# Kernel optimization log

Hardware: AMD Instinct MI355X
Metric: run time of the kernel (lower is better)

The kernel has to match this reference:

```python
import jax, jax.numpy as jnp
import numpy as np

NUM_GRAPHS = 2048


def gcn_conv(x, W, b, edge, N):
    # PyG GCNConv: x' = D^{-1/2} (A + I) D^{-1/2} (x W) + b
    src, dst = edge[0], edge[1]
    loop = jnp.arange(N, dtype=src.dtype)
    src = jnp.concatenate([src, loop])
    dst = jnp.concatenate([dst, loop])
    h = x @ W  # [N, out]
    deg = jax.ops.segment_sum(jnp.ones(dst.shape, x.dtype), dst, num_segments=N)
    dinv = jnp.where(deg > 0, jax.lax.rsqrt(deg), 0.0)
    norm = dinv[src] * dinv[dst]  # [E+N]
    out = jax.ops.segment_sum(h[src] * norm[:, None], dst, num_segments=N)
    return out + b


def pool_max_mean(x, batch, G):
    mx = jax.ops.segment_max(x, batch, num_segments=G)
    mx = jnp.where(jnp.isfinite(mx), mx, 0.0)  # guard empty segments
    s = jax.ops.segment_sum(x, batch, num_segments=G)
    cnt = jax.ops.segment_sum(jnp.ones((x.shape[0],), x.dtype), batch, num_segments=G)
    mean = s / jnp.maximum(cnt, 1.0)[:, None]
    return mx, mean


def setup_inputs() -> dict:
    key = jax.random.key(0)
    ks = jax.random.split(key, 20)
    F, CE, SE, DD = 64, 64, 32, 128
    Nc, Ec, Ns, Es = 100000, 1250000, 100000, 1250000

    def glorot(k, shape):
        fan_in, fan_out = shape[0], shape[1]
        lim = np.sqrt(6.0 / (fan_in + fan_out)).astype(np.float32)
        return jax.random.uniform(k, shape, jnp.float32, -lim, lim)

    inp = {
        "c": jax.random.normal(ks[0], (Nc, F), jnp.float32),
        "c_edge": jax.random.randint(ks[1], (2, Ec), 0, Nc),
        "c_batch": jnp.sort(jax.random.randint(ks[2], (Nc,), 0, NUM_GRAPHS)),
        "s": jax.random.normal(ks[3], (Ns, F), jnp.float32),
        "s_edge": jax.random.randint(ks[4], (2, Es), 0, Ns),
        "s_batch": jnp.sort(jax.random.randint(ks[5], (Ns,), 0, NUM_GRAPHS)),
        "Wc0": glorot(ks[6], (F, CE)), "bc0": jnp.zeros((CE,), jnp.float32),
        "Wc1": glorot(ks[7], (CE, CE)), "bc1": jnp.zeros((CE,), jnp.float32),
        "Wc2": glorot(ks[8], (CE, CE)), "bc2": jnp.zeros((CE,), jnp.float32),
        "Ws0": glorot(ks[9], (F, SE)), "bs0": jnp.zeros((SE,), jnp.float32),
        "Ws1": glorot(ks[10], (SE, SE)), "bs1": jnp.zeros((SE,), jnp.float32),
        "Ws2": glorot(ks[11], (SE, SE)), "bs2": jnp.zeros((SE,), jnp.float32),
        "Wd": glorot(ks[12], ((CE + SE) * 2, DD)), "bd": jnp.zeros((DD,), jnp.float32),
        "Wo": glorot(ks[13], (DD, 1)), "bo": jnp.zeros((1,), jnp.float32),
    }
    return inp


def reference(c, c_edge, c_batch, s, s_edge, s_batch,
              Wc0, bc0, Wc1, bc1, Wc2, bc2,
              Ws0, bs0, Ws1, bs1, Ws2, bs2,
              Wd, bd, Wo, bo):
    Nc, Ns = c.shape[0], s.shape[0]
    cro = jax.nn.relu(gcn_conv(c, Wc0, bc0, c_edge, Nc))
    cro = jax.nn.relu(gcn_conv(cro, Wc1, bc1, c_edge, Nc))
    cro = jax.nn.relu(gcn_conv(cro, Wc2, bc2, c_edge, Nc))
    solv = jax.nn.relu(gcn_conv(s, Ws0, bs0, s_edge, Ns))
    solv = jax.nn.relu(gcn_conv(solv, Ws1, bs1, s_edge, Ns))
    solv = jax.nn.relu(gcn_conv(solv, Ws2, bs2, s_edge, Ns))
    c_mx, c_mean = pool_max_mean(cro, c_batch, NUM_GRAPHS)
    s_mx, s_mean = pool_max_mean(solv, s_batch, NUM_GRAPHS)
    embed = jnp.concatenate([c_mx, c_mean, s_mx, s_mean], axis=1)  # [G, 192]
    dense = jax.nn.relu(embed @ Wd + bd)
    out = dense @ Wo + bo  # [G, 1]
    return out, embed
```

## Files before the change

kernel.cpp:

```cpp
#include <hip/hip_runtime.h>
#include <hip/hip_fp16.h>
#include <math.h>


static inline int cdiv(int a, int b) { return (a + b - 1) / b; }

#define BUCKET_CAP 8192
#define P1_CHUNK   4096

typedef _Float16 v8h __attribute__((ext_vector_type(8)));
typedef float    v4f __attribute__((ext_vector_type(4)));

__global__ void zero_int(int* __restrict__ p, int n) {
    int i = blockIdx.x * blockDim.x + threadIdx.x;
    if (i < n) p[i] = 0;
}

__global__ __launch_bounds__(256) void p1_partition(const int* __restrict__ c_edge, int Ec,
                                                    const int* __restrict__ s_edge, int Es,
                                                    int Nc_pad, int Etot, int nbuck,
                                                    int* __restrict__ bucket_fill,
                                                    unsigned* __restrict__ pk) {
    __shared__ unsigned       wbuf[P1_CHUNK];
    __shared__ unsigned short bbuf[P1_CHUNK];
    __shared__ int            hist[512];
    int e0 = blockIdx.x * P1_CHUNK;
    int n  = Etot - e0;
    if (n > P1_CHUNK) n = P1_CHUNK;
    for (int i = threadIdx.x; i < nbuck; i += 256) hist[i] = 0;
    __syncthreads();
    for (int i = threadIdx.x; i < n; i += 256) {
        int e = e0 + i, src, g;
        if (e < Ec) { src = c_edge[e]; g = c_edge[Ec + e]; }
        else        { int e2 = e - Ec; src = s_edge[e2]; g = Nc_pad + s_edge[Es + e2]; }
        int b   = g >> 9;
        wbuf[i] = ((unsigned)(g & 511) << 17) | (unsigned)src;
        bbuf[i] = (unsigned short)b;
        atomicAdd(&hist[b], 1);
    }
    __syncthreads();
    for (int i = threadIdx.x; i < nbuck; i += 256) {
        int h = hist[i];
        hist[i] = h ? atomicAdd(&bucket_fill[i], h) : 0;
    }
    __syncthreads();
    for (int i = threadIdx.x; i < n; i += 256) {
        int b    = bbuf[i];
        int slot = atomicAdd(&hist[b], 1);
        if (slot < BUCKET_CAP) pk[(size_t)b * BUCKET_CAP + slot] = wbuf[i];
    }
}

__global__ __launch_bounds__(512) void p2_scanbuckets(const int* __restrict__ fill, int nbuck,
                                                      int* __restrict__ basearr,
                                                      int* __restrict__ off_all, int Ntot_pad, int Etot) {
    __shared__ int sh[512];
    int v = (threadIdx.x < nbuck) ? fill[threadIdx.x] : 0;
    sh[threadIdx.x] = v;
    __syncthreads();
    for (int ofs = 1; ofs < 512; ofs <<= 1) {
        int t = (threadIdx.x >= ofs) ? sh[threadIdx.x - ofs] : 0;
        __syncthreads();
        sh[threadIdx.x] += t;
        __syncthreads();
    }
    if (threadIdx.x < nbuck) basearr[threadIdx.x] = sh[threadIdx.x] - v;
    if (threadIdx.x == 0) off_all[Ntot_pad] = Etot;
}

__global__ __launch_bounds__(512) void p3_build(const unsigned* __restrict__ pk,
                                                const int* __restrict__ fillarr,
                                                const int* __restrict__ basearr,
                                                int* __restrict__ off_all,
                                                float* __restrict__ dinv,
                                                int* __restrict__ csr) {
    __shared__ int sh[512];
    int b    = blockIdx.x;
    int fill = fillarr[b];
    if (fill > BUCKET_CAP) fill = BUCKET_CAP;
    int base = basearr[b];
    const unsigned* reg = pk + (size_t)b * BUCKET_CAP;
    sh[threadIdx.x] = 0;
    __syncthreads();
    for (int i = threadIdx.x; i < fill; i += 512) atomicAdd(&sh[reg[i] >> 17], 1);
    __syncthreads();
    int cnt = sh[threadIdx.x];
    for (int ofs = 1; ofs < 512; ofs <<= 1) {
        int t = (threadIdx.x >= ofs) ? sh[threadIdx.x - ofs] : 0;
        __syncthreads();
        sh[threadIdx.x] += t;
        __syncthreads();
    }
    int excl = sh[threadIdx.x] - cnt;
    int node = b * 512 + threadIdx.x;
    off_all[node] = base + excl;
    dinv[node]    = rsqrtf((float)(cnt + 1));
    __syncthreads();
    sh[threadIdx.x] = excl;
    __syncthreads();
    for (int i = threadIdx.x; i < fill; i += 512) {
        unsigned w    = reg[i];
        int      slot = atomicAdd(&sh[w >> 17], 1);
        csr[base + slot] = (int)(w & 0x1FFFFu);
    }
}

template <int K, int M, typename TIN>
__device__ void gemm_mfma(int bid, const TIN* __restrict__ X, const float* __restrict__ W,
                          const float* __restrict__ dinv, __half* __restrict__ H, int N,
                          char* smem_) {
    constexpr int RB = 64;
    constexpr int KP = K + 8;
    constexpr int NT = M / 16;
    constexpr int KS = K / 32;
    _Float16* Xh = (_Float16*)smem_;
    _Float16* Wz = Xh + RB * KP;
    const int t    = threadIdx.x;
    const int row0 = bid * RB;

    constexpr int WENT = NT * KS * 64;
    for (int idx = t; idx < WENT; idx += 256) {
        int lane = idx & 63, rest = idx >> 6;
        int ks = rest % KS, ntl = rest / KS;
        int kbase = ks * 32 + (lane >> 4) * 8;
        int col   = ntl * 16 + (lane & 15);
        union { float4 f4; _Float16 h[8]; } u;
#pragma unroll
        for (int j = 0; j < 8; ++j) u.h[j] = (_Float16)W[(kbase + j) * M + col];
        *(float4*)(Wz + idx * 8) = u.f4;
    }
    if constexpr (sizeof(TIN) == 4) {
        constexpr int NI = RB * K / 4;
        for (int idx = t; idx < NI; idx += 256) {
            int row = idx / (K / 4), k4 = idx % (K / 4);
            int gr = row0 + row;
            float4 v = make_float4(0.f, 0.f, 0.f, 0.f);
            if (gr < N) v = *(const float4*)((const float*)X + (size_t)gr * K + k4 * 4);
            union { float2 f2; _Float16 h[4]; } u;
            u.h[0] = (_Float16)v.x; u.h[1] = (_Float16)v.y;
            u.h[2] = (_Float16)v.z; u.h[3] = (_Float16)v.w;
            *(float2*)(Xh + row * KP + k4 * 4) = u.f2;
        }
    } else {
        constexpr int NI = RB * K / 8;
        for (int idx = t; idx < NI; idx += 256) {
            int row = idx / (K / 8), k8 = idx % (K / 8);
            int gr = row0 + row;
            float4 v = make_float4(0.f, 0.f, 0.f, 0.f);
            if (gr < N) v = *(const float4*)((const __half*)X + (size_t)gr * K + k8 * 8);
            *(float4*)(Xh + row * KP + k8 * 8) = v;
        }
    }
    __syncthreads();

    const int wave = t >> 6, lane = t & 63;
    const int quad = lane >> 4, nl = lane & 15;
    const int rowA = wave * 16 + nl;

    v4f acc[NT];
#pragma unroll
    for (int i = 0; i < NT; ++i) acc[i] = (v4f){0.f, 0.f, 0.f, 0.f};

#pragma unroll
    for (int ks = 0; ks < KS; ++ks) {
        v8h a = *(const v8h*)(Xh + rowA * KP + ks * 32 + quad * 8);
#pragma unroll
        for (int ntl = 0; ntl < NT; ++ntl) {
            v8h b = *(const v8h*)(Wz + ((ntl * KS + ks) * 64 + lane) * 8);
            acc[ntl] = __builtin_amdgcn_mfma_f32_16x16x32_f16(a, b, acc[ntl], 0, 0, 0);
        }
    }

#pragma unroll
    for (int r = 0; r < 4; ++r) {
        int gr = row0 + wave * 16 + quad * 4 + r;
        if (gr < N) {
            float dv = dinv[gr];
#pragma unroll
            for (int ntl = 0; ntl < NT; ++ntl)
                H[(size_t)gr * M + ntl * 16 + nl] = __float2half(acc[ntl][r] * dv);
        }
    }
}

__device__ __forceinline__ float4 load4h(const float2* __restrict__ base, size_t idx) {
    float2 r = base[idx];
    union { float2 f2; __half2 h2[2]; } u;
    u.f2 = r;
    float2 a = __half22float2(u.h2[0]);
    float2 b = __half22float2(u.h2[1]);
    return make_float4(a.x, a.y, b.x, b.y);
}

template <int M>
__device__ void agg_body(int bid, const __half* __restrict__ H,
                         const int* __restrict__ off_g,
                         const int* __restrict__ csr,
                         const float* __restrict__ dinv_g,
                         const float* __restrict__ b,
                         __half* __restrict__ out, int Nloc) {
    constexpr int L   = M / 4;
    constexpr int NPW = 64 / L;
    int lane = threadIdx.x & 63;
    int wave = threadIdx.x >> 6;
    int fq   = lane & (L - 1);
    int sub  = lane / L;
    int node = (bid * 4 + wave) * NPW + sub;
    if (node >= Nloc) return;
    const float2* H4 = (const float2*)H;
    int j0 = off_g[node], j1 = off_g[node + 1];
    float4 acc = load4h(H4, (size_t)node * L + fq);
    int j = j0;
    for (; j + 8 <= j1; j += 8) {
        int s0 = csr[j],     s1 = csr[j + 1], s2 = csr[j + 2], s3 = csr[j + 3];
        int s4 = csr[j + 4], s5 = csr[j + 5], s6 = csr[j + 6], s7 = csr[j + 7];
        float4 a0 = load4h(H4, (size_t)s0 * L + fq);
        float4 a1 = load4h(H4, (size_t)s1 * L + fq);
        float4 a2 = load4h(H4, (size_t)s2 * L + fq);
        float4 a3 = load4h(H4, (size_t)s3 * L + fq);
        float4 a4 = load4h(H4, (size_t)s4 * L + fq);
        float4 a5 = load4h(H4, (size_t)s5 * L + fq);
        float4 a6 = load4h(H4, (size_t)s6 * L + fq);
        float4 a7 = load4h(H4, (size_t)s7 * L + fq);
        acc.x += (a0.x + a1.x + a2.x + a3.x) + (a4.x + a5.x + a6.x + a7.x);
        acc.y += (a0.y + a1.y + a2.y + a3.y) + (a4.y + a5.y + a6.y + a7.y);
        acc.z += (a0.z + a1.z + a2.z + a3.z) + (a4.z + a5.z + a6.z + a7.z);
        acc.w += (a0.w + a1.w + a2.w + a3.w) + (a4.w + a5.w + a6.w + a7.w);
    }
    for (; j + 4 <= j1; j += 4) {
        int s0 = csr[j], s1 = csr[j + 1], s2 = csr[j + 2], s3 = csr[j + 3];
        float4 a0 = load4h(H4, (size_t)s0 * L + fq);
        float4 a1 = load4h(H4, (size_t)s1 * L + fq);
        float4 a2 = load4h(H4, (size_t)s2 * L + fq);
        float4 a3 = load4h(H4, (size_t)s3 * L + fq);
        acc.x += a0.x + a1.x + a2.x + a3.x;
        acc.y += a0.y + a1.y + a2.y + a3.y;
        acc.z += a0.z + a1.z + a2.z + a3.z;
        acc.w += a0.w + a1.w + a2.w + a3.w;
    }
    for (; j < j1; ++j) {
        float4 a = load4h(H4, (size_t)csr[j] * L + fq);
        acc.x += a.x; acc.y += a.y; acc.z += a.z; acc.w += a.w;
    }
    float  dv = dinv_g[node];
    float4 bb = ((const float4*)b)[fq];
    float  vx = dv * acc.x + bb.x;
    float  vy = dv * acc.y + bb.y;
    float  vz = dv * acc.z + bb.z;
    float  vw = dv * acc.w + bb.w;
    union { float2 f2; __half2 h2[2]; } o;
    o.h2[0] = __floats2half2_rn(vx > 0.f ? vx : 0.f, vy > 0.f ? vy : 0.f);
    o.h2[1] = __floats2half2_rn(vz > 0.f ? vz : 0.f, vw > 0.f ? vw : 0.f);
    ((float2*)out)[(size_t)node * L + fq] = o.f2;
}

__global__ __launch_bounds__(256) void gemmBoth0(const float* __restrict__ Xc, const float* __restrict__ Wc,
                                                 __half* __restrict__ cH, int Nc,
                                                 const float* __restrict__ Xs, const float* __restrict__ Ws,
                                                 __half* __restrict__ sH, int Ns,
                                                 const float* __restrict__ dinv_all, int Nc_pad, int nbC) {
    __shared__ __align__(16) char smem[17408];
    if (blockIdx.x < nbC) gemm_mfma<64, 64, float>(blockIdx.x, Xc, Wc, dinv_all, cH, Nc, smem);
    else                  gemm_mfma<64, 32, float>(blockIdx.x - nbC, Xs, Ws, dinv_all + Nc_pad, sH, Ns, smem);
}

__global__ __launch_bounds__(256) void gemmBoth(const __half* __restrict__ Xc, const float* __restrict__ Wc,
                                                __half* __restrict__ cH, int Nc,
                                                const __half* __restrict__ Xs, const float* __restrict__ Ws,
                                                __half* __restrict__ sH, int Ns,
                                                const float* __restrict__ dinv_all, int Nc_pad, int nbC) {
    __shared__ __align__(16) char smem[17408];
    if (blockIdx.x < nbC) gemm_mfma<64, 64, __half>(blockIdx.x, Xc, Wc, dinv_all, cH, Nc, smem);
    else                  gemm_mfma<32, 32, __half>(blockIdx.x - nbC, Xs, Ws, dinv_all + Nc_pad, sH, Ns, smem);
}

__global__ __launch_bounds__(256) void aggBoth(const __half* __restrict__ cH, const __half* __restrict__ sH,
                                               const int* __restrict__ off_all, const int* __restrict__ csr_all,
                                               const float* __restrict__ dinv_all,
                                               const float* __restrict__ bc, const float* __restrict__ bs,
                                               __half* __restrict__ outc, __half* __restrict__ outs,
                                               int Nc, int Ns, int Nc_pad, int nbC) {
    if (blockIdx.x < nbC)
        agg_body<64>(blockIdx.x, cH, off_all, csr_all, dinv_all, bc, outc, Nc);
    else
        agg_body<32>(blockIdx.x - nbC, sH, off_all + Nc_pad, csr_all,
                     dinv_all + Nc_pad, bs, outs, Ns);
}

__device__ __forceinline__ int lbound(const int* __restrict__ a, int n, int key) {
    int lo = 0, hi = n;
    while (lo < hi) {
        int mid = (lo + hi) >> 1;
        if (a[mid] < key) lo = mid + 1; else hi = mid;
    }
    return lo;
}

__global__ __launch_bounds__(128) void poolDense(const __half* __restrict__ cX, const int* __restrict__ c_batch, int Nc,
                                                 const __half* __restrict__ sX, const int* __restrict__ s_batch, int Ns,
                                                 const float* __restrict__ Wd, const float* __restrict__ bd,
                                                 const float* __restrict__ Wo, const float* __restrict__ bo,
                                                 float* __restrict__ outv, float* __restrict__ embed) {
    __shared__ float e[192];
    __shared__ float red[128];
    int g = blockIdx.x, t = threadIdx.x;
    if (t < 64) {
        int lo = lbound(c_batch, Nc, g), hi = lbound(c_batch, Nc, g + 1);
        float mx = 0.f, sm = 0.f;
        for (int i = lo; i < hi; ++i) {
            float v = __half2float(cX[(size_t)i * 64 + t]);
            mx = fmaxf(mx, v); sm += v;
        }
        int cn = hi - lo;
        e[t]      = mx;
        e[64 + t] = sm / (float)(cn > 0 ? cn : 1);
    } else if (t < 96) {
        int f  = t - 64;
        int lo = lbound(s_batch, Ns, g), hi = lbound(s_batch, Ns, g + 1);
        float mx = 0.f, sm = 0.f;
        for (int i = lo; i < hi; ++i) {
            float v = __half2float(sX[(size_t)i * 32 + f]);
            mx = fmaxf(mx, v); sm += v;
        }
        int cn = hi - lo;
        e[128 + f] = mx;
        e[160 + f] = sm / (float)(cn > 0 ? cn : 1);
    }
    __syncthreads();
    for (int k = t; k < 192; k += 128) embed[(size_t)g * 192 + k] = e[k];
    float acc = bd[t];
    for (int k = 0; k < 192; ++k) acc += e[k] * Wd[k * 128 + t];
    float d = acc > 0.f ? acc : 0.f;
    red[t]  = d * Wo[t];
    __syncthreads();
    for (int ofs = 64; ofs > 0; ofs >>= 1) {
        if (t < ofs) red[t] += red[t + ofs];
        __syncthreads();
    }
    if (t == 0) outv[g] = red[0] + bo[0];
}


extern "C" void kernel_launch(void* const* d_in, const int* in_sizes, int n_in,
                              void* d_out, int out_size, void* d_ws, size_t ws_size,
                              hipStream_t stream) {
    const float* c       = (const float*)d_in[0];
    const int*   c_edge  = (const int*)d_in[1];
    const int*   c_batch = (const int*)d_in[2];
    const float* s       = (const float*)d_in[3];
    const int*   s_edge  = (const int*)d_in[4];
    const int*   s_batch = (const int*)d_in[5];
    const float* Wc0 = (const float*)d_in[6],  *bc0 = (const float*)d_in[7];
    const float* Wc1 = (const float*)d_in[8],  *bc1 = (const float*)d_in[9];
    const float* Wc2 = (const float*)d_in[10], *bc2 = (const float*)d_in[11];
    const float* Ws0 = (const float*)d_in[12], *bs0 = (const float*)d_in[13];
    const float* Ws1 = (const float*)d_in[14], *bs1 = (const float*)d_in[15];
    const float* Ws2 = (const float*)d_in[16], *bs2 = (const float*)d_in[17];
    const float* Wd  = (const float*)d_in[18], *bd  = (const float*)d_in[19];
    const float* Wo  = (const float*)d_in[20], *bo  = (const float*)d_in[21];

    const int Nc = in_sizes[0] / 64;
    const int Ec = in_sizes[1] / 2;
    const int Ns = in_sizes[3] / 64;
    const int Es = in_sizes[4] / 2;
    const int G  = out_size / 193;
    const int Nc_pad   = cdiv(Nc, 512) * 512;
    const int Ns_pad   = cdiv(Ns, 512) * 512;
    const int Ntot_pad = Nc_pad + Ns_pad;
    const int Etot     = Ec + Es;
    const int nbuck    = Ntot_pad >> 9;

    char* p = (char*)d_ws;
    auto  alloc = [&](size_t bytes) -> void* {
        void* r = (void*)p;
        p += (bytes + 255) & ~(size_t)255;
        return r;
    };
    int*      bucket_fill = (int*)alloc(512 * 4);
    int*      bucket_base = (int*)alloc(512 * 4);
    unsigned* pk          = (unsigned*)alloc((size_t)nbuck * BUCKET_CAP * 4);
    int*      off_all     = (int*)alloc(((size_t)Ntot_pad + 1) * 4);
    int*      csr_all     = (int*)alloc((size_t)Etot * 4);
    float*    dinv_all    = (float*)alloc((size_t)Ntot_pad * 4);
    __half*   bufC        = (__half*)alloc((size_t)Nc * 64 * 2);
    __half*   bufS        = (__half*)alloc((size_t)Ns * 32 * 2);
    __half*   cH          = (__half*)alloc((size_t)Nc * 64 * 2);
    __half*   sH          = (__half*)alloc((size_t)Ns * 32 * 2);

    float* outv  = (float*)d_out;
    float* embed = outv + G;

    const int nbGmC = cdiv(Nc, 64), nbGmS = cdiv(Ns, 64);
    const int nbAgC = Nc_pad / 16,  nbAgS = Ns_pad / 32;

    zero_int<<<cdiv(nbuck, 256), 256, 0, stream>>>(bucket_fill, nbuck);
    p1_partition<<<cdiv(Etot, P1_CHUNK), 256, 0, stream>>>(c_edge, Ec, s_edge, Es,
                                                           Nc_pad, Etot, nbuck, bucket_fill, pk);
    p2_scanbuckets<<<1, 512, 0, stream>>>(bucket_fill, nbuck, bucket_base, off_all, Ntot_pad, Etot);
    p3_build<<<nbuck, 512, 0, stream>>>(pk, bucket_fill, bucket_base,
                                        off_all, dinv_all, csr_all);

    gemmBoth0<<<nbGmC + nbGmS, 256, 0, stream>>>(c, Wc0, cH, Nc, s, Ws0, sH, Ns,
                                                 dinv_all, Nc_pad, nbGmC);
    aggBoth<<<nbAgC + nbAgS, 256, 0, stream>>>(cH, sH, off_all, csr_all, dinv_all,
                                               bc0, bs0, bufC, bufS, Nc, Ns, Nc_pad, nbAgC);
    gemmBoth<<<nbGmC + nbGmS, 256, 0, stream>>>(bufC, Wc1, cH, Nc, bufS, Ws1, sH, Ns,
                                                dinv_all, Nc_pad, nbGmC);
    aggBoth<<<nbAgC + nbAgS, 256, 0, stream>>>(cH, sH, off_all, csr_all, dinv_all,
                                               bc1, bs1, bufC, bufS, Nc, Ns, Nc_pad, nbAgC);
    gemmBoth<<<nbGmC + nbGmS, 256, 0, stream>>>(bufC, Wc2, cH, Nc, bufS, Ws2, sH, Ns,
                                                dinv_all, Nc_pad, nbGmC);
    aggBoth<<<nbAgC + nbAgS, 256, 0, stream>>>(cH, sH, off_all, csr_all, dinv_all,
                                               bc2, bs2, bufC, bufS, Nc, Ns, Nc_pad, nbAgC);

    poolDense<<<G, 128, 0, stream>>>(bufC, c_batch, Nc, bufS, s_batch, Ns,
                                     Wd, bd, Wo, bo, outv, embed);
}
```

Measured before the change: 367.6 us.

## Fold bucket scan into CSR build and widen aggregation gathers to 16 bytes

The single-block bucket prefix scan kernel is removed, and every p3_build block now recomputes the bucket scan itself, saving one launch and its serialization at the cost of redundant scan work per block. The aggregation kernel switches from 8-byte to 16-byte half-precision gathers: each lane handles 8 features, so fewer lanes serve each node and more nodes fit per wave. The grid sizes are halved to match. The 8-way unrolled neighbor loop is dropped in favour of a 4-way loop, which lowers memory-level parallelism per lane but fits the wider loads.

```diff
diff --git a/kernel.cpp b/kernel.cpp
--- a/kernel.cpp
+++ b/kernel.cpp
@@ -51,54 +51,51 @@
     }
 }
 
-__global__ __launch_bounds__(512) void p2_scanbuckets(const int* __restrict__ fill, int nbuck,
-                                                      int* __restrict__ basearr,
-                                                      int* __restrict__ off_all, int Ntot_pad, int Etot) {
-    __shared__ int sh[512];
-    int v = (threadIdx.x < nbuck) ? fill[threadIdx.x] : 0;
-    sh[threadIdx.x] = v;
-    __syncthreads();
-    for (int ofs = 1; ofs < 512; ofs <<= 1) {
-        int t = (threadIdx.x >= ofs) ? sh[threadIdx.x - ofs] : 0;
-        __syncthreads();
-        sh[threadIdx.x] += t;
-        __syncthreads();
-    }
-    if (threadIdx.x < nbuck) basearr[threadIdx.x] = sh[threadIdx.x] - v;
-    if (threadIdx.x == 0) off_all[Ntot_pad] = Etot;
-}
-
 __global__ __launch_bounds__(512) void p3_build(const unsigned* __restrict__ pk,
                                                 const int* __restrict__ fillarr,
-                                                const int* __restrict__ basearr,
+                                                int nbuck, int Ntot_pad, int Etot,
                                                 int* __restrict__ off_all,
                                                 float* __restrict__ dinv,
                                                 int* __restrict__ csr) {
     __shared__ int sh[512];
-    int b    = blockIdx.x;
-    int fill = fillarr[b];
+    int b = blockIdx.x, tid = threadIdx.x;
+
+    int fv = (tid < nbuck) ? fillarr[tid] : 0;
+    sh[tid] = fv;
+    __syncthreads();
+    for (int ofs = 1; ofs < 512; ofs <<= 1) {
+        int t = (tid >= ofs) ? sh[tid - ofs] : 0;
+        __syncthreads();
+        sh[tid] += t;
+        __syncthreads();
+    }
+    int fill_b = fillarr[b];
+    int base   = sh[b] - fill_b;
+    if (b == 0 && tid == 0) off_all[Ntot_pad] = Etot;
+    int fill = fill_b;
     if (fill > BUCKET_CAP) fill = BUCKET_CAP;
-    int base = basearr[b];
     const unsigned* reg = pk + (size_t)b * BUCKET_CAP;
-    sh[threadIdx.x] = 0;
-    __syncthreads();
-    for (int i = threadIdx.x; i < fill; i += 512) atomicAdd(&sh[reg[i] >> 17], 1);
-    __syncthreads();
-    int cnt = sh[threadIdx.x];
+    __syncthreads();
+
+    sh[tid] = 0;
+    __syncthreads();
+    for (int i = tid; i < fill; i += 512) atomicAdd(&sh[reg[i] >> 17], 1);
+    __syncthreads();
+    int cnt = sh[tid];
     for (int ofs = 1; ofs < 512; ofs <<= 1) {
-        int t = (threadIdx.x >= ofs) ? sh[threadIdx.x - ofs] : 0;
+        int t = (tid >= ofs) ? sh[tid - ofs] : 0;
         __syncthreads();
-        sh[threadIdx.x] += t;
+        sh[tid] += t;
         __syncthreads();
     }
-    int excl = sh[threadIdx.x] - cnt;
-    int node = b * 512 + threadIdx.x;
+    int excl = sh[tid] - cnt;
+    int node = b * 512 + tid;
     off_all[node] = base + excl;
     dinv[node]    = rsqrtf((float)(cnt + 1));
     __syncthreads();
-    sh[threadIdx.x] = excl;
-    __syncthreads();
-    for (int i = threadIdx.x; i < fill; i += 512) {
+    sh[tid] = excl;
+    __syncthreads();
+    for (int i = tid; i < fill; i += 512) {
         unsigned w    = reg[i];
         int      slot = atomicAdd(&sh[w >> 17], 1);
         csr[base + slot] = (int)(w & 0x1FFFFu);
@@ -109,10 +106,7 @@
 __device__ void gemm_mfma(int bid, const TIN* __restrict__ X, const float* __restrict__ W,
                           const float* __restrict__ dinv, __half* __restrict__ H, int N,
                           char* smem_) {
-    constexpr int RB = 64;
-    constexpr int KP = K + 8;
-    constexpr int NT = M / 16;
-    constexpr int KS = K / 32;
+    constexpr int RB = 64, KP = K + 8, NT = M / 16, KS = K / 32;
     _Float16* Xh = (_Float16*)smem_;
     _Float16* Wz = Xh + RB * KP;
     const int t    = threadIdx.x;
@@ -160,7 +154,6 @@
     v4f acc[NT];
 #pragma unroll
     for (int i = 0; i < NT; ++i) acc[i] = (v4f){0.f, 0.f, 0.f, 0.f};
-
 #pragma unroll
     for (int ks = 0; ks < KS; ++ks) {
         v8h a = *(const v8h*)(Xh + rowA * KP + ks * 32 + quad * 8);
@@ -170,7 +163,6 @@
             acc[ntl] = __builtin_amdgcn_mfma_f32_16x16x32_f16(a, b, acc[ntl], 0, 0, 0);
         }
     }
-
 #pragma unroll
     for (int r = 0; r < 4; ++r) {
         int gr = row0 + wave * 16 + quad * 4 + r;
@@ -183,23 +175,28 @@
     }
 }
 
-__device__ __forceinline__ float4 load4h(const float2* __restrict__ base, size_t idx) {
-    float2 r = base[idx];
-    union { float2 f2; __half2 h2[2]; } u;
-    u.f2 = r;
-    float2 a = __half22float2(u.h2[0]);
-    float2 b = __half22float2(u.h2[1]);
-    return make_float4(a.x, a.y, b.x, b.y);
+__device__ __forceinline__ void cvt8h(float4 r, float4& lo, float4& hi) {
+    union { float4 f4; __half2 h2[4]; } u;
+    u.f4 = r;
+    float2 p0 = __half22float2(u.h2[0]);
+    float2 p1 = __half22float2(u.h2[1]);
+    float2 p2 = __half22float2(u.h2[2]);
+    float2 p3 = __half22float2(u.h2[3]);
+    lo = make_float4(p0.x, p0.y, p1.x, p1.y);
+    hi = make_float4(p2.x, p2.y, p3.x, p3.y);
+}
+
+__device__ __forceinline__ void add8(float4& alo, float4& ahi, float4 r4lo, float4 r4hi) {
+    alo.x += r4lo.x; alo.y += r4lo.y; alo.z += r4lo.z; alo.w += r4lo.w;
+    ahi.x += r4hi.x; ahi.y += r4hi.y; ahi.z += r4hi.z; ahi.w += r4hi.w;
 }
 
 template <int M>
 __device__ void agg_body(int bid, const __half* __restrict__ H,
-                         const int* __restrict__ off_g,
-                         const int* __restrict__ csr,
-                         const float* __restrict__ dinv_g,
-                         const float* __restrict__ b,
+                         const int* __restrict__ off_g, const int* __restrict__ csr,
+                         const float* __restrict__ dinv_g, const float* __restrict__ b,
                          __half* __restrict__ out, int Nloc) {
-    constexpr int L   = M / 4;
+    constexpr int L = M / 8;
     constexpr int NPW = 64 / L;
     int lane = threadIdx.x & 63;
     int wave = threadIdx.x >> 6;
@@ -207,51 +204,45 @@
     int sub  = lane / L;
     int node = (bid * 4 + wave) * NPW + sub;
     if (node >= Nloc) return;
-    const float2* H4 = (const float2*)H;
+    const float4* H8 = (const float4*)H;
     int j0 = off_g[node], j1 = off_g[node + 1];
-    float4 acc = load4h(H4, (size_t)node * L + fq);
+    float4 alo, ahi;
+    cvt8h(H8[(size_t)node * L + fq], alo, ahi);
     int j = j0;
-    for (; j + 8 <= j1; j += 8) {
-        int s0 = csr[j],     s1 = csr[j + 1], s2 = csr[j + 2], s3 = csr[j + 3];
-        int s4 = csr[j + 4], s5 = csr[j + 5], s6 = csr[j + 6], s7 = csr[j + 7];
-        float4 a0 = load4h(H4, (size_t)s0 * L + fq);
-        float4 a1 = load4h(H4, (size_t)s1 * L + fq);
-        float4 a2 = load4h(H4, (size_t)s2 * L + fq);
-        float4 a3 = load4h(H4, (size_t)s3 * L + fq);
-        float4 a4 = load4h(H4, (size_t)s4 * L + fq);
-        float4 a5 = load4h(H4, (size_t)s5 * L + fq);
-        float4 a6 = load4h(H4, (size_t)s6 * L + fq);
-        float4 a7 = load4h(H4, (size_t)s7 * L + fq);
-        acc.x += (a0.x + a1.x + a2.x + a3.x) + (a4.x + a5.x + a6.x + a7.x);
-        acc.y += (a0.y + a1.y + a2.y + a3.y) + (a4.y + a5.y + a6.y + a7.y);
-        acc.z += (a0.z + a1.z + a2.z + a3.z) + (a4.z + a5.z + a6.z + a7.z);
-        acc.w += (a0.w + a1.w + a2.w + a3.w) + (a4.w + a5.w + a6.w + a7.w);
-    }
     for (; j + 4 <= j1; j += 4) {
         int s0 = csr[j], s1 = csr[j + 1], s2 = csr[j + 2], s3 = csr[j + 3];
-        float4 a0 = load4h(H4, (size_t)s0 * L + fq);
-        float4 a1 = load4h(H4, (size_t)s1 * L + fq);
-        float4 a2 = load4h(H4, (size_t)s2 * L + fq);
-        float4 a3 = load4h(H4, (size_t)s3 * L + fq);
-        acc.x += a0.x + a1.x + a2.x + a3.x;
-        acc.y += a0.y + a1.y + a2.y + a3.y;
-        acc.z += a0.z + a1.z + a2.z + a3.z;
-        acc.w += a0.w + a1.w + a2.w + a3.w;
+        float4 r0 = H8[(size_t)s0 * L + fq];
+        float4 r1 = H8[(size_t)s1 * L + fq];
+        float4 r2 = H8[(size_t)s2 * L + fq];
+        float4 r3 = H8[(size_t)s3 * L + fq];
+        float4 lo, hi;
+        cvt8h(r0, lo, hi); add8(alo, ahi, lo, hi);
+        cvt8h(r1, lo, hi); add8(alo, ahi, lo, hi);
+        cvt8h(r2, lo, hi); add8(alo, ahi, lo, hi);
+        cvt8h(r3, lo, hi); add8(alo, ahi, lo, hi);
     }
     for (; j < j1; ++j) {
-        float4 a = load4h(H4, (size_t)csr[j] * L + fq);
-        acc.x += a.x; acc.y += a.y; acc.z += a.z; acc.w += a.w;
-    }
-    float  dv = dinv_g[node];
-    float4 bb = ((const float4*)b)[fq];
-    float  vx = dv * acc.x + bb.x;
-    float  vy = dv * acc.y + bb.y;
-    float  vz = dv * acc.z + bb.z;
-    float  vw = dv * acc.w + bb.w;
-    union { float2 f2; __half2 h2[2]; } o;
-    o.h2[0] = __floats2half2_rn(vx > 0.f ? vx : 0.f, vy > 0.f ? vy : 0.f);
-    o.h2[1] = __floats2half2_rn(vz > 0.f ? vz : 0.f, vw > 0.f ? vw : 0.f);
-    ((float2*)out)[(size_t)node * L + fq] = o.f2;
+        float4 lo, hi;
+        cvt8h(H8[(size_t)csr[j] * L + fq], lo, hi);
+        add8(alo, ahi, lo, hi);
+    }
+    float  dv  = dinv_g[node];
+    const float4* b4 = (const float4*)b;
+    float4 blo = b4[2 * fq], bhi = b4[2 * fq + 1];
+    float v0 = fmaxf(dv * alo.x + blo.x, 0.f);
+    float v1 = fmaxf(dv * alo.y + blo.y, 0.f);
+    float v2 = fmaxf(dv * alo.z + blo.z, 0.f);
+    float v3 = fmaxf(dv * alo.w + blo.w, 0.f);
+    float v4 = fmaxf(dv * ahi.x + bhi.x, 0.f);
+    float v5 = fmaxf(dv * ahi.y + bhi.y, 0.f);
+    float v6 = fmaxf(dv * ahi.z + bhi.z, 0.f);
+    float v7 = fmaxf(dv * ahi.w + bhi.w, 0.f);
+    union { float4 f4; __half2 h2[4]; } o;
+    o.h2[0] = __floats2half2_rn(v0, v1);
+    o.h2[1] = __floats2half2_rn(v2, v3);
+    o.h2[2] = __floats2half2_rn(v4, v5);
+    o.h2[3] = __floats2half2_rn(v6, v7);
+    ((float4*)out)[(size_t)node * L + fq] = o.f4;
 }
 
 __global__ __launch_bounds__(256) void gemmBoth0(const float* __restrict__ Xc, const float* __restrict__ Wc,
@@ -377,40 +368,38 @@
         return r;
     };
     int*      bucket_fill = (int*)alloc(512 * 4);
-    int*      bucket_base = (int*)alloc(512 * 4);
     unsigned* pk          = (unsigned*)alloc((size_t)nbuck * BUCKET_CAP * 4);
     int*      off_all     = (int*)alloc(((size_t)Ntot_pad + 1) * 4);
     int*      csr_all     = (int*)alloc((size_t)Etot * 4);
     float*    dinv_all    = (float*)alloc((size_t)Ntot_pad * 4);
     __half*   bufC        = (__half*)alloc((size_t)Nc * 64 * 2);
     __half*   bufS        = (__half*)alloc((size_t)Ns * 32 * 2);
-    __half*   cH          = (__half*)alloc((size_t)Nc * 64 * 2);
-    __half*   sH          = (__half*)alloc((size_t)Ns * 32 * 2);
+    __half*   cHa         = (__half*)alloc((size_t)Nc * 64 * 2);
+    __half*   sHa         = (__half*)alloc((size_t)Ns * 32 * 2);
 
     float* outv  = (float*)d_out;
     float* embed = outv + G;
 
     const int nbGmC = cdiv(Nc, 64), nbGmS = cdiv(Ns, 64);
-    const int nbAgC = Nc_pad / 16,  nbAgS = Ns_pad / 32;
+    const int nbAgC = Nc_pad / 32,  nbAgS = Ns_pad / 64;
 
     zero_int<<<cdiv(nbuck, 256), 256, 0, stream>>>(bucket_fill, nbuck);
     p1_partition<<<cdiv(Etot, P1_CHUNK), 256, 0, stream>>>(c_edge, Ec, s_edge, Es,
                                                            Nc_pad, Etot, nbuck, bucket_fill, pk);
-    p2_scanbuckets<<<1, 512, 0, stream>>>(bucket_fill, nbuck, bucket_base, off_all, Ntot_pad, Etot);
-    p3_build<<<nbuck, 512, 0, stream>>>(pk, bucket_fill, bucket_base,
+    p3_build<<<nbuck, 512, 0, stream>>>(pk, bucket_fill, nbuck, Ntot_pad, Etot,
                                         off_all, dinv_all, csr_all);
 
-    gemmBoth0<<<nbGmC + nbGmS, 256, 0, stream>>>(c, Wc0, cH, Nc, s, Ws0, sH, Ns,
+    gemmBoth0<<<nbGmC + nbGmS, 256, 0, stream>>>(c, Wc0, cHa, Nc, s, Ws0, sHa, Ns,
                                                  dinv_all, Nc_pad, nbGmC);
-    aggBoth<<<nbAgC + nbAgS, 256, 0, stream>>>(cH, sH, off_all, csr_all, dinv_all,
+    aggBoth<<<nbAgC + nbAgS, 256, 0, stream>>>(cHa, sHa, off_all, csr_all, dinv_all,
                                                bc0, bs0, bufC, bufS, Nc, Ns, Nc_pad, nbAgC);
-    gemmBoth<<<nbGmC + nbGmS, 256, 0, stream>>>(bufC, Wc1, cH, Nc, bufS, Ws1, sH, Ns,
+    gemmBoth<<<nbGmC + nbGmS, 256, 0, stream>>>(bufC, Wc1, cHa, Nc, bufS, Ws1, sHa, Ns,
                                                 dinv_all, Nc_pad, nbGmC);
-    aggBoth<<<nbAgC + nbAgS, 256, 0, stream>>>(cH, sH, off_all, csr_all, dinv_all,
+    aggBoth<<<nbAgC + nbAgS, 256, 0, stream>>>(cHa, sHa, off_all, csr_all, dinv_all,
                                                bc1, bs1, bufC, bufS, Nc, Ns, Nc_pad, nbAgC);
-    gemmBoth<<<nbGmC + nbGmS, 256, 0, stream>>>(bufC, Wc2, cH, Nc, bufS, Ws2, sH, Ns,
+    gemmBoth<<<nbGmC + nbGmS, 256, 0, stream>>>(bufC, Wc2, cHa, Nc, bufS, Ws2, sHa, Ns,
                                                 dinv_all, Nc_pad, nbGmC);
-    aggBoth<<<nbAgC + nbAgS, 256, 0, stream>>>(cH, sH, off_all, csr_all, dinv_all,
+    aggBoth<<<nbAgC + nbAgS, 256, 0, stream>>>(cHa, sHa, off_all, csr_all, dinv_all,
                                                bc2, bs2, bufC, bufS, Nc, Ns, Nc_pad, nbAgC);
 
     poolDense<<<G, 128, 0, stream>>>(bufC, c_batch, Nc, bufS, s_batch, Ns,
```

Measured after the change: 374.3 us. About the same (+1.8%).

## Overlap first-layer GEMM with edge partitioning and apply dinv scaling in CSR build

Applied to the files above, without the earlier changes.

The first-layer GEMM no longer depends on the degree normalisation. It is merged into one launch with the edge-partition pass so the two independent workloads run concurrently, and the separate gemmBoth0 launch is removed. The p3_build kernel then rescales the fp16 H rows in place by dinv after computing degrees. This adds an extra read-modify-write of H and a second fp16 rounding in exchange for one fewer launch and better overlap.

```diff
diff --git a/kernel.cpp b/kernel.cpp
--- a/kernel.cpp
+++ b/kernel.cpp
@@ -16,15 +16,15 @@
     if (i < n) p[i] = 0;
 }
 
-__global__ __launch_bounds__(256) void p1_partition(const int* __restrict__ c_edge, int Ec,
-                                                    const int* __restrict__ s_edge, int Es,
-                                                    int Nc_pad, int Etot, int nbuck,
-                                                    int* __restrict__ bucket_fill,
-                                                    unsigned* __restrict__ pk) {
-    __shared__ unsigned       wbuf[P1_CHUNK];
-    __shared__ unsigned short bbuf[P1_CHUNK];
-    __shared__ int            hist[512];
-    int e0 = blockIdx.x * P1_CHUNK;
+__device__ void p1_body(int bid, const int* __restrict__ c_edge, int Ec,
+                        const int* __restrict__ s_edge, int Es,
+                        int Nc_pad, int Etot, int nbuck,
+                        int* __restrict__ bucket_fill, unsigned* __restrict__ pk,
+                        char* smem_) {
+    unsigned*       wbuf = (unsigned*)smem_;
+    unsigned short* bbuf = (unsigned short*)(smem_ + 16384);
+    int*            hist = (int*)(smem_ + 24576);
+    int e0 = bid * P1_CHUNK;
     int n  = Etot - e0;
     if (n > P1_CHUNK) n = P1_CHUNK;
     for (int i = threadIdx.x; i < nbuck; i += 256) hist[i] = 0;
@@ -73,35 +73,78 @@
                                                 const int* __restrict__ basearr,
                                                 int* __restrict__ off_all,
                                                 float* __restrict__ dinv,
-                                                int* __restrict__ csr) {
-    __shared__ int sh[512];
+                                                int* __restrict__ csr,
+                                                __half* __restrict__ cH, __half* __restrict__ sH,
+                                                int Nc, int Ns, int Nc_pad, int nbuckC) {
+    __shared__ int   sh[512];
+    __shared__ float dls[512];
     int b    = blockIdx.x;
+    int tid  = threadIdx.x;
     int fill = fillarr[b];
     if (fill > BUCKET_CAP) fill = BUCKET_CAP;
     int base = basearr[b];
     const unsigned* reg = pk + (size_t)b * BUCKET_CAP;
-    sh[threadIdx.x] = 0;
-    __syncthreads();
-    for (int i = threadIdx.x; i < fill; i += 512) atomicAdd(&sh[reg[i] >> 17], 1);
-    __syncthreads();
-    int cnt = sh[threadIdx.x];
+    sh[tid] = 0;
+    __syncthreads();
+    for (int i = tid; i < fill; i += 512) atomicAdd(&sh[reg[i] >> 17], 1);
+    __syncthreads();
+    int cnt = sh[tid];
     for (int ofs = 1; ofs < 512; ofs <<= 1) {
-        int t = (threadIdx.x >= ofs) ? sh[threadIdx.x - ofs] : 0;
+        int t = (tid >= ofs) ? sh[tid - ofs] : 0;
         __syncthreads();
-        sh[threadIdx.x] += t;
+        sh[tid] += t;
         __syncthreads();
     }
-    int excl = sh[threadIdx.x] - cnt;
-    int node = b * 512 + threadIdx.x;
+    int excl = sh[tid] - cnt;
+    int node = b * 512 + tid;
+    float dv = rsqrtf((float)(cnt + 1));
     off_all[node] = base + excl;
-    dinv[node]    = rsqrtf((float)(cnt + 1));
-    __syncthreads();
-    sh[threadIdx.x] = excl;
-    __syncthreads();
-    for (int i = threadIdx.x; i < fill; i += 512) {
+    dinv[node]    = dv;
+    dls[tid]      = dv;
+    __syncthreads();
+    sh[tid] = excl;
+    __syncthreads();
+    for (int i = tid; i < fill; i += 512) {
         unsigned w    = reg[i];
         int      slot = atomicAdd(&sh[w >> 17], 1);
         csr[base + slot] = (int)(w & 0x1FFFFu);
+    }
+    if (b < nbuckC) {
+        int rbase = b * 512;
+        float4* H4 = (float4*)cH;
+        for (int idx = tid; idx < 512 * 8; idx += 512) {
+            int rl = idx >> 3, ch = idx & 7;
+            int row = rbase + rl;
+            if (row < Nc) {
+                float d = dls[rl];
+                union { float4 f4; __half2 h2[4]; } u;
+                u.f4 = H4[(size_t)row * 8 + ch];
+#pragma unroll
+                for (int q = 0; q < 4; ++q) {
+                    float2 p = __half22float2(u.h2[q]);
+                    u.h2[q]  = __floats2half2_rn(p.x * d, p.y * d);
+                }
+                H4[(size_t)row * 8 + ch] = u.f4;
+            }
+        }
+    } else {
+        int rbase = b * 512 - Nc_pad;
+        float4* H4 = (float4*)sH;
+        for (int idx = tid; idx < 512 * 4; idx += 512) {
+            int rl = idx >> 2, ch = idx & 3;
+            int row = rbase + rl;
+            if (row < Ns) {
+                float d = dls[rl];
+                union { float4 f4; __half2 h2[4]; } u;
+                u.f4 = H4[(size_t)row * 4 + ch];
+#pragma unroll
+                for (int q = 0; q < 4; ++q) {
+                    float2 p = __half22float2(u.h2[q]);
+                    u.h2[q]  = __floats2half2_rn(p.x * d, p.y * d);
+                }
+                H4[(size_t)row * 4 + ch] = u.f4;
+            }
+        }
     }
 }
 
@@ -109,10 +152,7 @@
 __device__ void gemm_mfma(int bid, const TIN* __restrict__ X, const float* __restrict__ W,
                           const float* __restrict__ dinv, __half* __restrict__ H, int N,
                           char* smem_) {
-    constexpr int RB = 64;
-    constexpr int KP = K + 8;
-    constexpr int NT = M / 16;
-    constexpr int KS = K / 32;
+    constexpr int RB = 64, KP = K + 8, NT = M / 16, KS = K / 32;
     _Float16* Xh = (_Float16*)smem_;
     _Float16* Wz = Xh + RB * KP;
     const int t    = threadIdx.x;
@@ -160,7 +200,6 @@
     v4f acc[NT];
 #pragma unroll
     for (int i = 0; i < NT; ++i) acc[i] = (v4f){0.f, 0.f, 0.f, 0.f};
-
 #pragma unroll
     for (int ks = 0; ks < KS; ++ks) {
         v8h a = *(const v8h*)(Xh + rowA * KP + ks * 32 + quad * 8);
@@ -170,12 +209,11 @@
             acc[ntl] = __builtin_amdgcn_mfma_f32_16x16x32_f16(a, b, acc[ntl], 0, 0, 0);
         }
     }
-
 #pragma unroll
     for (int r = 0; r < 4; ++r) {
         int gr = row0 + wave * 16 + quad * 4 + r;
         if (gr < N) {
-            float dv = dinv[gr];
+            float dv = dinv ? dinv[gr] : 1.0f;
 #pragma unroll
             for (int ntl = 0; ntl < NT; ++ntl)
                 H[(size_t)gr * M + ntl * 16 + nl] = __float2half(acc[ntl][r] * dv);
@@ -194,13 +232,10 @@
 
 template <int M>
 __device__ void agg_body(int bid, const __half* __restrict__ H,
-                         const int* __restrict__ off_g,
-                         const int* __restrict__ csr,
-                         const float* __restrict__ dinv_g,
-                         const float* __restrict__ b,
+                         const int* __restrict__ off_g, const int* __restrict__ csr,
+                         const float* __restrict__ dinv_g, const float* __restrict__ b,
                          __half* __restrict__ out, int Nloc) {
-    constexpr int L   = M / 4;
-    constexpr int NPW = 64 / L;
+    constexpr int L = M / 4, NPW = 64 / L;
     int lane = threadIdx.x & 63;
     int wave = threadIdx.x >> 6;
     int fq   = lane & (L - 1);
@@ -254,14 +289,22 @@
     ((float2*)out)[(size_t)node * L + fq] = o.f2;
 }
 
-__global__ __launch_bounds__(256) void gemmBoth0(const float* __restrict__ Xc, const float* __restrict__ Wc,
-                                                 __half* __restrict__ cH, int Nc,
-                                                 const float* __restrict__ Xs, const float* __restrict__ Ws,
-                                                 __half* __restrict__ sH, int Ns,
-                                                 const float* __restrict__ dinv_all, int Nc_pad, int nbC) {
-    __shared__ __align__(16) char smem[17408];
-    if (blockIdx.x < nbC) gemm_mfma<64, 64, float>(blockIdx.x, Xc, Wc, dinv_all, cH, Nc, smem);
-    else                  gemm_mfma<64, 32, float>(blockIdx.x - nbC, Xs, Ws, dinv_all + Nc_pad, sH, Ns, smem);
+__global__ __launch_bounds__(256) void phaseA(const int* __restrict__ c_edge, int Ec,
+                                              const int* __restrict__ s_edge, int Es,
+                                              int Nc_pad, int Etot, int nbuck,
+                                              int* __restrict__ bucket_fill, unsigned* __restrict__ pk,
+                                              const float* __restrict__ c, const float* __restrict__ Wc0,
+                                              __half* __restrict__ cH, int Nc,
+                                              const float* __restrict__ s, const float* __restrict__ Ws0,
+                                              __half* __restrict__ sH, int Ns,
+                                              int nbP1, int nbGmC) {
+    __shared__ __align__(16) char smem[26624];
+    int b = blockIdx.x;
+    if (b < nbP1) { p1_body(b, c_edge, Ec, s_edge, Es, Nc_pad, Etot, nbuck, bucket_fill, pk, smem); return; }
+    b -= nbP1;
+    if (b < nbGmC) { gemm_mfma<64, 64, float>(b, c, Wc0, nullptr, cH, Nc, smem); return; }
+    b -= nbGmC;
+    gemm_mfma<64, 32, float>(b, s, Ws0, nullptr, sH, Ns, smem);
 }
 
 __global__ __launch_bounds__(256) void gemmBoth(const __half* __restrict__ Xc, const float* __restrict__ Wc,
@@ -369,6 +412,7 @@
     const int Ntot_pad = Nc_pad + Ns_pad;
     const int Etot     = Ec + Es;
     const int nbuck    = Ntot_pad >> 9;
+    const int nbuckC   = Nc_pad >> 9;
 
     char* p = (char*)d_ws;
     auto  alloc = [&](size_t bytes) -> void* {
@@ -384,33 +428,34 @@
     float*    dinv_all    = (float*)alloc((size_t)Ntot_pad * 4);
     __half*   bufC        = (__half*)alloc((size_t)Nc * 64 * 2);
     __half*   bufS        = (__half*)alloc((size_t)Ns * 32 * 2);
-    __half*   cH          = (__half*)alloc((size_t)Nc * 64 * 2);
-    __half*   sH          = (__half*)alloc((size_t)Ns * 32 * 2);
+    __half*   cHa         = (__half*)alloc((size_t)Nc * 64 * 2);
+    __half*   sHa         = (__half*)alloc((size_t)Ns * 32 * 2);
 
     float* outv  = (float*)d_out;
     float* embed = outv + G;
 
+    const int nbP1  = cdiv(Etot, P1_CHUNK);
     const int nbGmC = cdiv(Nc, 64), nbGmS = cdiv(Ns, 64);
     const int nbAgC = Nc_pad / 16,  nbAgS = Ns_pad / 32;
 
     zero_int<<<cdiv(nbuck, 256), 256, 0, stream>>>(bucket_fill, nbuck);
-    p1_partition<<<cdiv(Etot, P1_CHUNK), 256, 0, stream>>>(c_edge, Ec, s_edge, Es,
-                                                           Nc_pad, Etot, nbuck, bucket_fill, pk);
+    phaseA<<<nbP1 + nbGmC + nbGmS, 256, 0, stream>>>(
+        c_edge, Ec, s_edge, Es, Nc_pad, Etot, nbuck, bucket_fill, pk,
+        c, Wc0, cHa, Nc, s, Ws0, sHa, Ns, nbP1, nbGmC);
     p2_scanbuckets<<<1, 512, 0, stream>>>(bucket_fill, nbuck, bucket_base, off_all, Ntot_pad, Etot);
     p3_build<<<nbuck, 512, 0, stream>>>(pk, bucket_fill, bucket_base,
-                                        off_all, dinv_all, csr_all);
-
-    gemmBoth0<<<nbGmC + nbGmS, 256, 0, stream>>>(c, Wc0, cH, Nc, s, Ws0, sH, Ns,
-                                                 dinv_all, Nc_pad, nbGmC);
-    aggBoth<<<nbAgC + nbAgS, 256, 0, stream>>>(cH, sH, off_all, csr_all, dinv_all,
+                                        off_all, dinv_all, csr_all,
+                                        cHa, sHa, Nc, Ns, Nc_pad, nbuckC);
+
+    aggBoth<<<nbAgC + nbAgS, 256, 0, stream>>>(cHa, sHa, off_all, csr_all, dinv_all,
                                                bc0, bs0, bufC, bufS, Nc, Ns, Nc_pad, nbAgC);
-    gemmBoth<<<nbGmC + nbGmS, 256, 0, stream>>>(bufC, Wc1, cH, Nc, bufS, Ws1, sH, Ns,
+    gemmBoth<<<nbGmC + nbGmS, 256, 0, stream>>>(bufC, Wc1, cHa, Nc, bufS, Ws1, sHa, Ns,
                                                 dinv_all, Nc_pad, nbGmC);
-    aggBoth<<<nbAgC + nbAgS, 256, 0, stream>>>(cH, sH, off_all, csr_all, dinv_all,
+    aggBoth<<<nbAgC + nbAgS, 256, 0, stream>>>(cHa, sHa, off_all, csr_all, dinv_all,
                                                bc1, bs1, bufC, bufS, Nc, Ns, Nc_pad, nbAgC);
-    gemmBoth<<<nbGmC + nbGmS, 256, 0, stream>>>(bufC, Wc2, cH, Nc, bufS, Ws2, sH, Ns,
+    gemmBoth<<<nbGmC + nbGmS, 256, 0, stream>>>(bufC, Wc2, cHa, Nc, bufS, Ws2, sHa, Ns,
                                                 dinv_all, Nc_pad, nbGmC);
-    aggBoth<<<nbAgC + nbAgS, 256, 0, stream>>>(cH, sH, off_all, csr_all, dinv_all,
+    aggBoth<<<nbAgC + nbAgS, 256, 0, stream>>>(cHa, sHa, off_all, csr_all, dinv_all,
                                                bc2, bs2, bufC, bufS, Nc, Ns, Nc_pad, nbAgC);
 
     poolDense<<<G, 128, 0, stream>>>(bufC, c_batch, Nc, bufS, s_batch, Ns,
```

New measurement: 369.5 us. About the same (+0.5%).
